# Kernel optimization log

Hardware: AMD Instinct MI355X
Metric: run time of the kernel (lower is better)

The kernel has to match this reference:

```python
import jax, jax.numpy as jnp
import numpy as np

NH = 16          # num_attention_heads
SMAX = 400.0     # smax for previous-task gates

def _gelu(x):
    return jax.nn.gelu(x, approximate=False)

def setup_inputs() -> dict:
    key = jax.random.key(0)
    ks = jax.random.split(key, 18)
    B, S, H, A, N = 8, 2048, 1024, 512, 10
    sc = lambda fan: 1.0 / np.sqrt(fan)
    f32 = jnp.float32
    return {
        "x":     jax.random.normal(ks[0], (B, S, H), f32),
        "fc1_w": jax.random.normal(ks[1], (A, H), f32) * sc(H),
        "fc1_b": jnp.zeros((A,), f32),
        "fc2_w": jax.random.normal(ks[2], (H, A), f32) * sc(A),
        "fc2_b": jnp.zeros((H,), f32),
        "efc1":  jax.random.normal(ks[3], (N, A), f32),
        "efc2":  jax.random.normal(ks[4], (N, H), f32),
        "etask": jax.random.normal(ks[5], (N, H), f32),
        "q_w":   jax.random.normal(ks[6], (H, H), f32) * sc(H),
        "q_b":   jnp.zeros((H,), f32),
        "k_w":   jax.random.normal(ks[7], (H, H), f32) * sc(H),
        "k_b":   jnp.zeros((H,), f32),
        "v_w":   jax.random.normal(ks[8], (H, H), f32) * sc(H),
        "v_b":   jnp.zeros((H,), f32),
        "equery": jax.random.normal(ks[9],  (N, H), f32),
        "ekey":   jax.random.normal(ks[10], (N, H), f32),
        "evalue": jax.random.normal(ks[11], (N, H), f32),
        "t": 5,
        "s": 400,
    }

def reference(x, fc1_w, fc1_b, fc2_w, fc2_b, efc1, efc2, etask,
              q_w, q_b, k_w, k_b, v_w, v_b, equery, ekey, evalue, t, s):
    B, S, H = x.shape
    hd = H // NH
    s = jnp.float32(s)

    # --- current-task gated adapter: h = act(fc2(act(fc1(x)) * gfc1)) * gfc2 ---
    h1 = _gelu(x @ fc1_w.T + fc1_b)                         # [B,S,A]
    gfc1 = jax.nn.sigmoid(s * efc1[t])                      # [A]
    gfc2 = jax.nn.sigmoid(s * efc2[t])                      # [H]
    h = _gelu((h1 * gfc1) @ fc2_w.T + fc2_b) * gfc2         # [B,S,H]

    # --- previous tasks (detached, gates at smax); vectorized over pre_t ---
    pg1 = jax.nn.sigmoid(SMAX * efc1[:t])                   # [t,A]
    pg2 = jax.nn.sigmoid(SMAX * efc2[:t])                   # [t,H]
    pre_h1 = h1[:, None, :, :] * pg1[None, :, None, :]      # [B,t,S,A]
    pre_h = _gelu(jnp.einsum('btsa,ha->btsh', pre_h1, fc2_w) + fc2_b)
    pre_h = jax.lax.stop_gradient(pre_h * pg2[None, :, None, :])  # [B,t,S,H]

    hid = jnp.concatenate([h[:, None], pre_h], axis=1)      # [B,T,S,H], T=t+1
    Tn = t + 1

    # --- task-gated QKV ---
    t_emb = jnp.broadcast_to(etask[t], (B, 1, S, H))        # query_states
    gq = jax.nn.sigmoid(s * equery[t])
    gk = jax.nn.sigmoid(s * ekey[t])
    gv = jax.nn.sigmoid(s * evalue[t])
    q = (t_emb @ q_w.T + q_b) * gq                          # [B,1,S,H]
    k = (hid @ k_w.T + k_b) * gk                            # [B,T,S,H]
    v = (hid @ v_w.T + v_b) * gv                            # [B,T,S,H]

    q5 = q.reshape(B, 1, S, NH, hd)
    k5 = k.reshape(B, Tn, S, NH, hd)
    v5 = v.reshape(B, Tn, S, NH, hd)

    # torch permute algebra: contract over heads (n), softmax over tasks (t)
    scores = jnp.einsum('bqsnd,btsnd->bdsqt', q5, k5) / np.sqrt(hd)  # [B,hd,S,1,T]
    probs = jax.nn.softmax(scores, axis=-1)
    ctx = jnp.einsum('bdsqt,btsnd->bdsqn', probs, v5)       # [B,hd,S,1,NH]
    ctx = ctx[:, :, :, 0, :].transpose(0, 2, 1, 3).reshape(B, S, H)

    return x + ctx
```

## Files before the change

kernel.cpp:

```cpp
#include <hip/hip_runtime.h>
#include <hip/hip_bf16.h>

static constexpr int B_ = 8, S_ = 2048, H_ = 1024, A_ = 512;
static constexpr int M_ = B_ * S_;
static constexpr int T_ = 6;
static constexpr long HID_STRIDE = (long)M_ * H_;
static constexpr long SC_STRIDE  = (long)M_ * 64;

typedef __attribute__((ext_vector_type(4))) float f32x4;
typedef __attribute__((ext_vector_type(8))) short bf16x8;

__device__ __forceinline__ float bf2f(ushort u){ return __uint_as_float(((unsigned)u) << 16); }
__device__ __forceinline__ ushort f2bf(float f){
  __hip_bfloat16 h = __float2bfloat16(f);
  return __builtin_bit_cast(unsigned short, h);
}
__device__ __forceinline__ float geluf(float x){
  return 0.5f * x * (1.0f + erff(x * 0.70710678118654752440f));
}
__device__ __forceinline__ float sigm(float x){ return 1.0f / (1.0f + __expf(-x)); }

__device__ __forceinline__ void gload_lds16(const void* g, void* l){
  __builtin_amdgcn_global_load_lds((const __attribute__((address_space(1))) void*)g,
                                   (__attribute__((address_space(3))) void*)l, 16, 0, 0);
}


__global__ void gates_kernel(const float* __restrict__ efc1, const float* __restrict__ efc2,
                             const int* __restrict__ tptr, const int* __restrict__ sptr,
                             float* __restrict__ g1, float* __restrict__ g2)
{
  const int h = threadIdx.x;
  const int t = *tptr;
  const float s = (float)(*sptr);
  #pragma unroll
  for (int ti = 0; ti < T_; ++ti) {
    const int task = (ti == 0) ? t : (ti - 1);
    const float scl = (ti == 0) ? s : 400.0f;
    g2[ti * H_ + h] = sigm(scl * efc2[task * H_ + h]);
    if (h < A_) g1[ti * A_ + h] = sigm(scl * efc1[task * A_ + h]);
  }
}

__global__ void kq_kernel(const float* __restrict__ etask, const float* __restrict__ q_w,
                          const float* __restrict__ q_b, const float* __restrict__ equery,
                          const float* __restrict__ ekey, const float* __restrict__ k_w,
                          const float* __restrict__ k_b,
                          const int* __restrict__ tptr, const int* __restrict__ sptr,
                          ushort* __restrict__ kqw, float* __restrict__ kqb)
{
  __shared__ float qg[16];
  const int d = blockIdx.x;
  const int tid = threadIdx.x;
  const int t = *tptr;
  const float s = (float)(*sptr);
  if (tid < 16) {
    const int hp = tid * 64 + d;
    const float* et = etask + (long)t * H_;
    const float* qw = q_w + (long)hp * H_;
    float acc = 0.f;
    for (int i = 0; i < H_; ++i) acc += et[i] * qw[i];
    float qv = (acc + q_b[hp]) * sigm(s * equery[t * H_ + hp]);
    qg[tid] = qv * sigm(s * ekey[t * H_ + hp]);
  }
  __syncthreads();
  for (int hh = tid; hh < H_; hh += 256) {
    float acc = 0.f;
    #pragma unroll
    for (int n = 0; n < 16; ++n) acc += qg[n] * k_w[(long)(n * 64 + d) * H_ + hh];
    kqw[d * H_ + hh] = f2bf(acc);
  }
  if (tid == 0) {
    float acc = 0.f;
    #pragma unroll
    for (int n = 0; n < 16; ++n) acc += qg[n] * k_b[n * 64 + d];
    kqb[d] = acc;
  }
}

__global__ void conv_bf16(const float* __restrict__ in, ushort* __restrict__ outp, long n)
{
  long i = ((long)blockIdx.x * blockDim.x + threadIdx.x) * 4;
  const long stride = (long)gridDim.x * blockDim.x * 4;
  for (; i < n; i += stride) {
    float4 v = *(const float4*)(in + i);
    ushort4 o;
    o.x = f2bf(v.x); o.y = f2bf(v.y); o.z = f2bf(v.z); o.w = f2bf(v.w);
    *(ushort4*)(outp + i) = o;
  }
}

__global__ void conv_w2g(const float* __restrict__ fc2w, const float* __restrict__ g1,
                         ushort* __restrict__ W2g)
{
  const long total = (long)T_ * H_ * A_;
  long i = ((long)blockIdx.x * blockDim.x + threadIdx.x) * 4;
  if (i >= total) return;
  const int ti = (int)(i / ((long)H_ * A_));
  const long r = i - (long)ti * H_ * A_;
  const int a = (int)(r & (A_ - 1));
  float4 wv = *(const float4*)(fc2w + r);
  const float* g = g1 + ti * A_ + a;
  ushort4 o;
  o.x = f2bf(wv.x * g[0]); o.y = f2bf(wv.y * g[1]);
  o.z = f2bf(wv.z * g[2]); o.w = f2bf(wv.w * g[3]);
  *(ushort4*)(W2g + i) = o;
}

__global__ void conv_vw(const float* __restrict__ v_w, const float* __restrict__ v_b,
                        const float* __restrict__ evalue,
                        const int* __restrict__ tptr, const int* __restrict__ sptr,
                        ushort* __restrict__ vwb, float* __restrict__ vbg)
{
  const int t = *tptr;
  const float s = (float)(*sptr);
  long i = ((long)blockIdx.x * blockDim.x + threadIdx.x) * 4;
  if (i < (long)H_ * H_) {
    const int f = (int)(i >> 10);
    const int hp = ((f & 15) << 6) + (f >> 4);
    const float g = sigm(s * evalue[t * H_ + hp]);
    float4 wv = *(const float4*)(v_w + ((long)hp << 10) + (i & 1023));
    ushort4 o;
    o.x = f2bf(wv.x * g); o.y = f2bf(wv.y * g);
    o.z = f2bf(wv.z * g); o.w = f2bf(wv.w * g);
    *(ushort4*)(vwb + i) = o;
  }
  const long j = (long)blockIdx.x * blockDim.x + threadIdx.x;
  if (j < H_) {
    const int hp = (((int)j & 15) << 6) + ((int)j >> 4);
    vbg[j] = v_b[hp] * sigm(s * evalue[t * H_ + hp]);
  }
}

template<int BM, int BN, int EPI>
__global__ __launch_bounds__(256)
void gemm_bt(const ushort* __restrict__ A, const ushort* __restrict__ Bm,
             void* __restrict__ C, const float* __restrict__ bias,
             const float* __restrict__ scale,
             int M, int N, int K,
             long strideAz, long strideBz, long strideCz, int strideSz,
             float postmul)
{
  constexpr int BK = 32;
  constexpr int WM = BM / 2, WN = BN / 2;
  constexpr int MI = WM / 16, NI = WN / 16;
  __shared__ alignas(16) ushort As[2][BM * BK];
  __shared__ alignas(16) ushort Bs[2][BN * BK];

  const int z = blockIdx.z;
  A  += (long)z * strideAz;
  Bm += (long)z * strideBz;

  const int gx = gridDim.x, gy = gridDim.y;
  int flat = blockIdx.y * gx + blockIdx.x;
  const int nwg = gx * gy;
  if ((nwg & 7) == 0) flat = (flat & 7) * (nwg >> 3) + (flat >> 3);
  const int m0 = (flat / gy) * BM, n0 = (flat % gy) * BN;

  const int tid = threadIdx.x, lane = tid & 63, wid = tid >> 6;
  const int wr = wid >> 1, wc = wid & 1;
  const int srow = tid >> 2;
  const int scol = (tid & 3) * 8;

  auto stage = [&](int buf, int kk) {
    #pragma unroll
    for (int i = 0; i < BM / 64; ++i)
      gload_lds16(A + (long)(m0 + i * 64 + srow) * K + kk + scol,
                  &As[buf][(i * 64 + srow) * BK + scol]);
    #pragma unroll
    for (int i = 0; i < BN / 64; ++i)
      gload_lds16(Bm + (long)(n0 + i * 64 + srow) * K + kk + scol,
                  &Bs[buf][(i * 64 + srow) * BK + scol]);
  };

  f32x4 acc[MI][NI] = {};

  stage(0, 0);
  asm volatile("s_waitcnt vmcnt(0)" ::: "memory");
  __syncthreads();

  int cur = 0;
  for (int kk = 0; kk < K; kk += BK) {
    if (kk + BK < K) stage(cur ^ 1, kk + BK);

    bf16x8 af[MI], bfr[NI];
    #pragma unroll
    for (int m = 0; m < MI; ++m)
      af[m] = *(const bf16x8*)&As[cur][(wr * WM + m * 16 + (lane & 15)) * BK + (lane >> 4) * 8];
    #pragma unroll
    for (int n = 0; n < NI; ++n)
      bfr[n] = *(const bf16x8*)&Bs[cur][(wc * WN + n * 16 + (lane & 15)) * BK + (lane >> 4) * 8];
    #pragma unroll
    for (int m = 0; m < MI; ++m)
      #pragma unroll
      for (int n = 0; n < NI; ++n)
        acc[m][n] = __builtin_amdgcn_mfma_f32_16x16x32_bf16(af[m], bfr[n], acc[m][n], 0, 0, 0);

    asm volatile("s_waitcnt vmcnt(0)" ::: "memory");
    __syncthreads();
    cur ^= 1;
  }

  const float* sc = (EPI == 1) ? (scale + (long)z * strideSz) : nullptr;
  #pragma unroll
  for (int m = 0; m < MI; ++m) {
    #pragma unroll
    for (int n = 0; n < NI; ++n) {
      const int col = n0 + wc * WN + n * 16 + (lane & 15);
      const float bv = bias[col];
      #pragma unroll
      for (int r = 0; r < 4; ++r) {
        const int row = m0 + wr * WM + m * 16 + (lane >> 4) * 4 + r;
        const float v = acc[m][n][r] + bv;
        const long ci = (long)z * strideCz + (long)row * N + col;
        if constexpr (EPI == 0) {
          ((ushort*)C)[ci] = f2bf(geluf(v));
        } else if constexpr (EPI == 1) {
          ((ushort*)C)[ci] = f2bf(geluf(v) * sc[col]);
        } else {
          ((float*)C)[ci] = v * postmul;
        }
      }
    }
  }
}

__global__ __launch_bounds__(256, 3)
void fusedv_kernel(const ushort* __restrict__ hidb, const ushort* __restrict__ vwb,
                   const float* __restrict__ scB, const float* __restrict__ vbg,
                   const float* __restrict__ x, float* __restrict__ out)
{
  constexpr int BM = 128, BN = 64, BK = 32;
  constexpr int WM = 64, WN = 32, MI = 4, NI = 2;
  __shared__ alignas(16) ushort As[2][BM * BK];
  __shared__ alignas(16) ushort Bs[2][BN * BK];
  __shared__ float p_lds[T_ * BM * 4];

  const int gx = gridDim.x, gy = gridDim.y;
  int flat = blockIdx.y * gx + blockIdx.x;
  const int nwg = gx * gy;
  flat = (flat & 7) * (nwg >> 3) + (flat >> 3);
  const int m0 = (flat / gy) * BM, n0 = (flat % gy) * BN;
  const int d0 = n0 >> 4;

  const int tid = threadIdx.x, lane = tid & 63, wid = tid >> 6;
  const int wr = wid >> 1, wc = wid & 1;
  const int srow = tid >> 2;
  const int scol = (tid & 3) * 8;

  auto stageAB = [&](int buf, int kt) {
    const int ti = kt >> 5;
    const int kk = (kt & 31) << 5;
    const ushort* Ap = hidb + (long)ti * HID_STRIDE;
    #pragma unroll
    for (int i = 0; i < 2; ++i)
      gload_lds16(Ap + (long)(m0 + i * 64 + srow) * H_ + kk + scol,
                  &As[buf][(i * 64 + srow) * BK + scol]);
    gload_lds16(vwb + (long)(n0 + srow) * H_ + kk + scol,
                &Bs[buf][srow * BK + scol]);
  };

  stageAB(0, 0);
  #pragma unroll
  for (int c = 0; c < 2; ++c) {
    const int cell = tid + c * 256;
    const int row = cell >> 2, dl = cell & 3;
    const long base = (long)(m0 + row) * 64 + d0 + dl;
    float v[T_]; float mx = -1e30f;
    #pragma unroll
    for (int ti = 0; ti < T_; ++ti) {
      v[ti] = scB[(long)ti * SC_STRIDE + base];
      mx = fmaxf(mx, v[ti]);
    }
    float sum = 0.f;
    #pragma unroll
    for (int ti = 0; ti < T_; ++ti) { v[ti] = __expf(v[ti] - mx); sum += v[ti]; }
    const float inv = 1.0f / sum;
    #pragma unroll
    for (int ti = 0; ti < T_; ++ti) p_lds[(ti * BM + row) * 4 + dl] = v[ti] * inv;
  }
  asm volatile("s_waitcnt vmcnt(0)" ::: "memory");
  __syncthreads();

  const f32x4 zero = {};
  f32x4 ctx[MI][NI] = {};
  f32x4 acc[MI][NI] = {};

  int cur = 0;
  for (int kt = 0; kt < T_ * 32; ++kt) {
    if (kt + 1 < T_ * 32) stageAB(cur ^ 1, kt + 1);

    bf16x8 af[MI], bfr[NI];
    #pragma unroll
    for (int m = 0; m < MI; ++m)
      af[m] = *(const bf16x8*)&As[cur][(wr * WM + m * 16 + (lane & 15)) * BK + (lane >> 4) * 8];
    #pragma unroll
    for (int n = 0; n < NI; ++n)
      bfr[n] = *(const bf16x8*)&Bs[cur][(wc * WN + n * 16 + (lane & 15)) * BK + (lane >> 4) * 8];
    #pragma unroll
    for (int m = 0; m < MI; ++m)
      #pragma unroll
      for (int n = 0; n < NI; ++n)
        acc[m][n] = __builtin_amdgcn_mfma_f32_16x16x32_bf16(af[m], bfr[n], acc[m][n], 0, 0, 0);

    if ((kt & 31) == 31) {
      const int ti = kt >> 5;
      #pragma unroll
      for (int m = 0; m < MI; ++m) {
        #pragma unroll
        for (int r = 0; r < 4; ++r) {
          const int rowl = wr * WM + m * 16 + (lane >> 4) * 4 + r;
          const float2 pv = *(const float2*)&p_lds[(ti * BM + rowl) * 4 + wc * 2];
          ctx[m][0][r] += pv.x * acc[m][0][r];
          ctx[m][1][r] += pv.y * acc[m][1][r];
        }
        acc[m][0] = zero; acc[m][1] = zero;
      }
    }

    asm volatile("s_waitcnt vmcnt(0)" ::: "memory");
    __syncthreads();
    cur ^= 1;
  }

  #pragma unroll
  for (int m = 0; m < MI; ++m) {
    #pragma unroll
    for (int n = 0; n < NI; ++n) {
      const int col = n0 + wc * WN + n * 16 + (lane & 15);
      const float bv = vbg[col];
      #pragma unroll
      for (int r = 0; r < 4; ++r) {
        const int row = m0 + wr * WM + m * 16 + (lane >> 4) * 4 + r;
        const long ci = (long)row * H_ + col;
        out[ci] = x[ci] + ctx[m][n][r] + bv;
      }
    }
  }
}

extern "C" void kernel_launch(void* const* d_in, const int* in_sizes, int n_in,
                              void* d_out, int out_size, void* d_ws, size_t ws_size,
                              hipStream_t stream)
{
  const float* x      = (const float*)d_in[0];
  const float* fc1_w  = (const float*)d_in[1];
  const float* fc1_b  = (const float*)d_in[2];
  const float* fc2_w  = (const float*)d_in[3];
  const float* fc2_b  = (const float*)d_in[4];
  const float* efc1   = (const float*)d_in[5];
  const float* efc2   = (const float*)d_in[6];
  const float* etask  = (const float*)d_in[7];
  const float* q_w    = (const float*)d_in[8];
  const float* q_b    = (const float*)d_in[9];
  const float* k_w    = (const float*)d_in[10];
  const float* k_b    = (const float*)d_in[11];
  const float* v_w    = (const float*)d_in[12];
  const float* v_b    = (const float*)d_in[13];
  const float* equery = (const float*)d_in[14];
  const float* ekey   = (const float*)d_in[15];
  const float* evalue = (const float*)d_in[16];
  const int*   tptr   = (const int*)d_in[17];
  const int*   sptr   = (const int*)d_in[18];
  float* out = (float*)d_out;

  char* w = (char*)d_ws;
  ushort* hidb = (ushort*)w; w += (long)T_ * M_ * H_ * 2;
  char* regionA = w;         w += (long)M_ * H_ * 2;
  ushort* xb  = (ushort*)regionA;
  float*  scB = (float*)regionA;
  ushort* h1b  = (ushort*)w; w += (long)M_ * A_ * 2;
  ushort* w1b  = (ushort*)w; w += (long)A_ * H_ * 2;
  ushort* W2g  = (ushort*)w; w += (long)T_ * H_ * A_ * 2;
  ushort* vwb  = (ushort*)w; w += (long)H_ * H_ * 2;
  ushort* kqw  = (ushort*)w; w += (long)64 * H_ * 2;
  float*  kqb  = (float*)w;  w += 64 * 4;
  float*  g1   = (float*)w;  w += T_ * A_ * 4;
  float*  g2   = (float*)w;  w += T_ * H_ * 4;
  float*  vbg  = (float*)w;  w += H_ * 4;
  (void)ws_size; (void)in_sizes; (void)n_in; (void)out_size;

  gates_kernel<<<1, 1024, 0, stream>>>(efc1, efc2, tptr, sptr, g1, g2);
  kq_kernel<<<64, 256, 0, stream>>>(etask, q_w, q_b, equery, ekey, k_w, k_b,
                                    tptr, sptr, kqw, kqb);
  conv_vw<<<1024, 256, 0, stream>>>(v_w, v_b, evalue, tptr, sptr, vwb, vbg);

  conv_bf16<<<2048, 256, 0, stream>>>(x, xb, (long)M_ * H_);
  conv_bf16<<<256, 256, 0, stream>>>(fc1_w, w1b, (long)A_ * H_);
  conv_w2g<<<3072, 256, 0, stream>>>(fc2_w, g1, W2g);

  gemm_bt<128, 128, 0><<<dim3(M_ / 128, A_ / 128, 1), 256, 0, stream>>>(
      xb, w1b, h1b, fc1_b, nullptr, M_, A_, H_, 0, 0, 0, 0, 0.f);

  gemm_bt<128, 128, 1><<<dim3(M_ / 128, H_ / 128, T_), 256, 0, stream>>>(
      h1b, W2g, hidb, fc2_b, g2, M_, H_, A_,
      0, (long)H_ * A_, HID_STRIDE, H_, 0.f);

  gemm_bt<128, 64, 2><<<dim3(M_ / 128, 1, T_), 256, 0, stream>>>(
      hidb, kqw, scB, kqb, nullptr, M_, 64, H_,
      HID_STRIDE, 0, SC_STRIDE, 0, 0.125f);

  fusedv_kernel<<<dim3(M_ / 128, H_ / 64, 1), 256, 0, stream>>>(
      hidb, vwb, scB, vbg, x, out);
}
```

Baseline: 682.7 us.

## Deepen GEMM prefetch to two stages with partial vmcnt waits and split barriers

Both the generic bf16 GEMM and the fused V/softmax kernel now keep two K-tiles of global→LDS loads in flight. Instead of waiting for all loads (vmcnt 0) each iteration, they wait with a partial vmcnt count that lets the newest tile's loads stay outstanding. Fragments are read into registers before the second barrier, which frees the buffer to be refilled immediately, and MFMA priority is raised via s_setprio. This is meant to hide global memory latency behind compute, at the cost of relying on hand-counted vmcnt values that must match the number of loads issued per stage.

New measurement: 612.2 us. 1.12x faster.

```diff
diff --git a/kernel.cpp b/kernel.cpp
--- a/kernel.cpp
+++ b/kernel.cpp
@@ -144,6 +144,7 @@
   constexpr int BK = 32;
   constexpr int WM = BM / 2, WN = BN / 2;
   constexpr int MI = WM / 16, NI = WN / 16;
+  constexpr int L = BM / 64 + BN / 64;
   __shared__ alignas(16) ushort As[2][BM * BK];
   __shared__ alignas(16) ushort Bs[2][BN * BK];
 
@@ -174,14 +175,21 @@
   };
 
   f32x4 acc[MI][NI] = {};
+  const int NT = K / BK;
 
   stage(0, 0);
-  asm volatile("s_waitcnt vmcnt(0)" ::: "memory");
-  __syncthreads();
+  stage(1, BK);
 
   int cur = 0;
-  for (int kk = 0; kk < K; kk += BK) {
-    if (kk + BK < K) stage(cur ^ 1, kk + BK);
+  for (int t = 0; t < NT; ++t) {
+    if (t + 1 < NT) {
+      if constexpr (L == 4) asm volatile("s_waitcnt vmcnt(4)" ::: "memory");
+      else                  asm volatile("s_waitcnt vmcnt(3)" ::: "memory");
+    } else {
+      asm volatile("s_waitcnt vmcnt(0)" ::: "memory");
+    }
+    __builtin_amdgcn_s_barrier();
+    __builtin_amdgcn_sched_barrier(0);
 
     bf16x8 af[MI], bfr[NI];
     #pragma unroll
@@ -190,14 +198,20 @@
     #pragma unroll
     for (int n = 0; n < NI; ++n)
       bfr[n] = *(const bf16x8*)&Bs[cur][(wc * WN + n * 16 + (lane & 15)) * BK + (lane >> 4) * 8];
+    asm volatile("s_waitcnt lgkmcnt(0)" ::: "memory");
+    __builtin_amdgcn_sched_barrier(0);
+    __builtin_amdgcn_s_barrier();
+    __builtin_amdgcn_sched_barrier(0);
+
+    if (t + 2 < NT) stage(cur, (t + 2) * BK);
+
+    __builtin_amdgcn_s_setprio(1);
     #pragma unroll
     for (int m = 0; m < MI; ++m)
       #pragma unroll
       for (int n = 0; n < NI; ++n)
         acc[m][n] = __builtin_amdgcn_mfma_f32_16x16x32_bf16(af[m], bfr[n], acc[m][n], 0, 0, 0);
-
-    asm volatile("s_waitcnt vmcnt(0)" ::: "memory");
-    __syncthreads();
+    __builtin_amdgcn_s_setprio(0);
     cur ^= 1;
   }
 
@@ -232,6 +246,7 @@
 {
   constexpr int BM = 128, BN = 64, BK = 32;
   constexpr int WM = 64, WN = 32, MI = 4, NI = 2;
+  constexpr int NT = T_ * 32;
   __shared__ alignas(16) ushort As[2][BM * BK];
   __shared__ alignas(16) ushort Bs[2][BN * BK];
   __shared__ float p_lds[T_ * BM * 4];
@@ -279,16 +294,19 @@
     #pragma unroll
     for (int ti = 0; ti < T_; ++ti) p_lds[(ti * BM + row) * 4 + dl] = v[ti] * inv;
   }
-  asm volatile("s_waitcnt vmcnt(0)" ::: "memory");
-  __syncthreads();
+  asm volatile("s_waitcnt lgkmcnt(0)" ::: "memory");
+  stageAB(1, 1);
 
   const f32x4 zero = {};
   f32x4 ctx[MI][NI] = {};
   f32x4 acc[MI][NI] = {};
 
   int cur = 0;
-  for (int kt = 0; kt < T_ * 32; ++kt) {
-    if (kt + 1 < T_ * 32) stageAB(cur ^ 1, kt + 1);
+  for (int kt = 0; kt < NT; ++kt) {
+    if (kt + 1 < NT) asm volatile("s_waitcnt vmcnt(3)" ::: "memory");
+    else             asm volatile("s_waitcnt vmcnt(0)" ::: "memory");
+    __builtin_amdgcn_s_barrier();
+    __builtin_amdgcn_sched_barrier(0);
 
     bf16x8 af[MI], bfr[NI];
     #pragma unroll
@@ -297,11 +315,20 @@
     #pragma unroll
     for (int n = 0; n < NI; ++n)
       bfr[n] = *(const bf16x8*)&Bs[cur][(wc * WN + n * 16 + (lane & 15)) * BK + (lane >> 4) * 8];
+    asm volatile("s_waitcnt lgkmcnt(0)" ::: "memory");
+    __builtin_amdgcn_sched_barrier(0);
+    __builtin_amdgcn_s_barrier();
+    __builtin_amdgcn_sched_barrier(0);
+
+    if (kt + 2 < NT) stageAB(cur, kt + 2);
+
+    __builtin_amdgcn_s_setprio(1);
     #pragma unroll
     for (int m = 0; m < MI; ++m)
       #pragma unroll
       for (int n = 0; n < NI; ++n)
         acc[m][n] = __builtin_amdgcn_mfma_f32_16x16x32_bf16(af[m], bfr[n], acc[m][n], 0, 0, 0);
+    __builtin_amdgcn_s_setprio(0);
 
     if ((kt & 31) == 31) {
       const int ti = kt >> 5;
@@ -317,9 +344,6 @@
         acc[m][0] = zero; acc[m][1] = zero;
       }
     }
-
-    asm volatile("s_waitcnt vmcnt(0)" ::: "memory");
-    __syncthreads();
     cur ^= 1;
   }
 
```
